# Optimization experiments

Hardware: AMD Instinct MI355X
Metric: run time of the kernel (lower is better)

## Reference

```python
import jax, jax.numpy as jnp
import numpy as np

B, N, F_IN = 4, 8000, 256
D_DIST = 128   # distance_dim
DFF = 128      # hidden width of both FFNs
BIN_SIZE = 500
NBINS = N // BIN_SIZE  # 16
K = 8          # num_neighbors
DIST_MULT = 0.1
MAX_NUM_BINS = 200


def setup_inputs() -> dict:
    key = jax.random.key(0)
    ks = jax.random.split(key, 8)
    s = 0.05
    return {
        "inputs": jax.random.normal(ks[0], (B, N, F_IN), jnp.float32),
        "enc_w1": jax.random.normal(ks[1], (F_IN, DFF), jnp.float32) * s,
        "enc_b1": jnp.zeros((DFF,), jnp.float32),
        "enc_w2": jax.random.normal(ks[2], (DFF, D_DIST), jnp.float32) * s,
        "enc_b2": jnp.zeros((D_DIST,), jnp.float32),
        "edge_w1": jax.random.normal(ks[3], (2 * F_IN + 1, DFF), jnp.float32) * s,
        "edge_b1": jnp.zeros((DFF,), jnp.float32),
        "edge_w2": jax.random.normal(ks[4], (DFF, 1), jnp.float32) * s,
        "edge_b2": jnp.zeros((1,), jnp.float32),
        "rot": jax.random.normal(ks[5], (D_DIST, MAX_NUM_BINS // 2), jnp.float32) * 0.05,
    }


def _per_batch(points, rot):
    # points: [N, D_DIST]. LSH bucketing via random rotations.
    mul = points @ rot[:, : NBINS // 2]                 # [N, NBINS//2]
    cmul = jnp.concatenate([mul, -mul], axis=-1)        # [N, NBINS]
    bin_idx = jnp.argmax(cmul, axis=-1)
    bins_split = jnp.argsort(bin_idx).astype(jnp.int32).reshape(NBINS, BIN_SIZE)
    parts = points[bins_split]                          # [NBINS, BIN_SIZE, D]
    # per-bin pairwise gaussian kernel
    na = jnp.sum(parts * parts, axis=-1)                # [NBINS, BIN_SIZE]
    d2 = na[:, :, None] - 2.0 * jnp.einsum('bnd,bmd->bnm', parts, parts) + na[:, None, :]
    dm = jnp.exp(-DIST_MULT * jnp.sqrt(jnp.maximum(d2, 1e-6)))  # [NBINS, BS, BS]
    vals, idx = jax.lax.top_k(dm, K)                    # [NBINS, BS, K]
    dst = jax.vmap(lambda b, i: b[i])(bins_split, idx)  # map in-bin idx -> global
    src = jnp.broadcast_to(bins_split[:, :, None], dst.shape)
    return src.reshape(-1), dst.reshape(-1), vals.reshape(-1), bins_split


def reference(inputs, enc_w1, enc_b1, enc_w2, enc_b2,
              edge_w1, edge_b1, edge_w2, edge_b2, rot):
    # point encoding FFN: Dense(128, elu) -> Dense(distance_dim)
    pe = jax.nn.elu(inputs @ enc_w1 + enc_b1) @ enc_w2 + enc_b2  # [B, N, D_DIST]
    src, dst, vals, bins_split = jax.vmap(_per_batch, in_axes=(0, None))(pe, rot)
    bidx = jnp.broadcast_to(jnp.arange(B, dtype=jnp.int32)[:, None], src.shape)
    src = src.reshape(-1)
    dst = dst.reshape(-1)
    vals = vals.reshape(-1)
    bidx = bidx.reshape(-1)
    # tf.sparse.reorder: canonical row-major ordering (no duplicates: top-k
    # indices are distinct per row and src is unique per neighbor slot)
    order = jnp.lexsort((dst, src, bidx))
    bidx, src, dst, vals = bidx[order], src[order], dst[order], vals[order]
    # edge network on gathered endpoint features + kernel value
    x1 = inputs[bidx, src]                               # [E, F_IN]
    x2 = inputs[bidx, dst]
    e = jnp.concatenate([x1, x2, vals[:, None]], axis=-1)  # [E, 2*F_IN+1]
    edge_vals = jax.nn.sigmoid(jax.nn.elu(e @ edge_w1 + edge_b1) @ edge_w2 + edge_b2)[:, 0]
    indices = jnp.stack([bidx, src, dst], axis=-1)       # [E, 3] sparse indices
    return indices, edge_vals, bins_split
```

## Files before the change

### kernel.cpp

```cpp
#include <hip/hip_runtime.h>
#include <math.h>

#define BB 4
#define NN 8000
#define FIN 256
#define DD 128
#define NB 16
#define BS 500
#define KK 8
#define RPB 32
#define CHUNKS (NN/RPB)
#define ETOT (BB*NN*KK)

__global__ __launch_bounds__(256) void k_fused(
    const float* __restrict__ x, const float* __restrict__ w1, const float* __restrict__ b1,
    const float* __restrict__ w2, const float* __restrict__ b2, const float* __restrict__ rot,
    const float* __restrict__ ew1,
    float* __restrict__ pe, float* __restrict__ A, float* __restrict__ Bv,
    int* __restrict__ bin_idx, int* __restrict__ localrank, int* __restrict__ chunkhist)
{
  __shared__ float wsa[32*132];
  __shared__ float wsb[32*132];
  __shared__ float ps[RPB*132];
  __shared__ float ms[RPB*9];
  __shared__ int   bl[RPB];
  const int t = threadIdx.x;
  const int b = blockIdx.x / CHUNKS;
  const int chunk = blockIdx.x % CHUNKS;
  const int row0 = chunk * RPB;
  const int ri = t >> 4;
  const int ci = t & 15;
  const int r0t = ri*2, r1t = ri*2+1;
  const float* xrow0 = x + ((size_t)b*NN + row0 + r0t)*FIN;
  const float* xrow1 = x + ((size_t)b*NN + row0 + r1t)*FIN;
  const int sk = t >> 5, sc4 = t & 31;

  float acc0[8], acc1[8];
  #pragma unroll
  for (int j=0;j<8;j++){ float bb = b1[ci*8+j]; acc0[j]=bb; acc1[j]=bb; }

  float4 rw0,rw1,rw2,rw3;
  { const float4* wg = (const float4*)w1;
    rw0=wg[t]; rw1=wg[t+256]; rw2=wg[t+512]; rw3=wg[t+768]; }
  int cur = 0;
  for (int kt=0; kt<8; ++kt){
    float* wsc = cur ? wsb : wsa;
    *(float4*)&wsc[(sk   )*132 + sc4*4] = rw0;
    *(float4*)&wsc[(sk+ 8)*132 + sc4*4] = rw1;
    *(float4*)&wsc[(sk+16)*132 + sc4*4] = rw2;
    *(float4*)&wsc[(sk+24)*132 + sc4*4] = rw3;
    if (kt<7){ const float4* wg = (const float4*)(w1 + (size_t)(kt+1)*32*DD);
      rw0=wg[t]; rw1=wg[t+256]; rw2=wg[t+512]; rw3=wg[t+768]; }
    __syncthreads();
    const float* xp0 = xrow0 + kt*32;
    const float* xp1 = xrow1 + kt*32;
    #pragma unroll
    for (int kc=0;kc<32;kc+=4){
      float4 a0 = *(const float4*)(xp0+kc);
      float4 a1 = *(const float4*)(xp1+kc);
      #pragma unroll
      for (int kk=0;kk<4;kk++){
        float4 wlo = *(const float4*)&wsc[(kc+kk)*132 + ci*8];
        float4 whi = *(const float4*)&wsc[(kc+kk)*132 + ci*8 + 4];
        float a0v = ((const float*)&a0)[kk], a1v = ((const float*)&a1)[kk];
        acc0[0]=fmaf(a0v,wlo.x,acc0[0]); acc0[1]=fmaf(a0v,wlo.y,acc0[1]);
        acc0[2]=fmaf(a0v,wlo.z,acc0[2]); acc0[3]=fmaf(a0v,wlo.w,acc0[3]);
        acc0[4]=fmaf(a0v,whi.x,acc0[4]); acc0[5]=fmaf(a0v,whi.y,acc0[5]);
        acc0[6]=fmaf(a0v,whi.z,acc0[6]); acc0[7]=fmaf(a0v,whi.w,acc0[7]);
        acc1[0]=fmaf(a1v,wlo.x,acc1[0]); acc1[1]=fmaf(a1v,wlo.y,acc1[1]);
        acc1[2]=fmaf(a1v,wlo.z,acc1[2]); acc1[3]=fmaf(a1v,wlo.w,acc1[3]);
        acc1[4]=fmaf(a1v,whi.x,acc1[4]); acc1[5]=fmaf(a1v,whi.y,acc1[5]);
        acc1[6]=fmaf(a1v,whi.z,acc1[6]); acc1[7]=fmaf(a1v,whi.w,acc1[7]);
      }
    }
    cur ^= 1;
  }
  #pragma unroll
  for (int j=0;j<8;j++){
    float v0=acc0[j]; ps[r0t*132 + ci*8 + j] = v0>0.f ? v0 : expm1f(v0);
    float v1=acc1[j]; ps[r1t*132 + ci*8 + j] = v1>0.f ? v1 : expm1f(v1);
  }

  float acc20[8], acc21[8];
  #pragma unroll
  for (int j=0;j<8;j++){ float bb = b2[ci*8+j]; acc20[j]=bb; acc21[j]=bb; }
  { const float4* wg = (const float4*)w2;
    rw0=wg[t]; rw1=wg[t+256]; rw2=wg[t+512]; rw3=wg[t+768]; }
  for (int kt=0; kt<4; ++kt){
    float* wsc = cur ? wsb : wsa;
    *(float4*)&wsc[(sk   )*132 + sc4*4] = rw0;
    *(float4*)&wsc[(sk+ 8)*132 + sc4*4] = rw1;
    *(float4*)&wsc[(sk+16)*132 + sc4*4] = rw2;
    *(float4*)&wsc[(sk+24)*132 + sc4*4] = rw3;
    if (kt<3){ const float4* wg = (const float4*)(w2 + (size_t)(kt+1)*32*DD);
      rw0=wg[t]; rw1=wg[t+256]; rw2=wg[t+512]; rw3=wg[t+768]; }
    __syncthreads();
    #pragma unroll
    for (int kc=0;kc<32;kc+=4){
      float4 a0 = *(const float4*)&ps[r0t*132 + kt*32 + kc];
      float4 a1 = *(const float4*)&ps[r1t*132 + kt*32 + kc];
      #pragma unroll
      for (int kk=0;kk<4;kk++){
        float4 wlo = *(const float4*)&wsc[(kc+kk)*132 + ci*8];
        float4 whi = *(const float4*)&wsc[(kc+kk)*132 + ci*8 + 4];
        float a0v = ((const float*)&a0)[kk], a1v = ((const float*)&a1)[kk];
        acc20[0]=fmaf(a0v,wlo.x,acc20[0]); acc20[1]=fmaf(a0v,wlo.y,acc20[1]);
        acc20[2]=fmaf(a0v,wlo.z,acc20[2]); acc20[3]=fmaf(a0v,wlo.w,acc20[3]);
        acc20[4]=fmaf(a0v,whi.x,acc20[4]); acc20[5]=fmaf(a0v,whi.y,acc20[5]);
        acc20[6]=fmaf(a0v,whi.z,acc20[6]); acc20[7]=fmaf(a0v,whi.w,acc20[7]);
        acc21[0]=fmaf(a1v,wlo.x,acc21[0]); acc21[1]=fmaf(a1v,wlo.y,acc21[1]);
        acc21[2]=fmaf(a1v,wlo.z,acc21[2]); acc21[3]=fmaf(a1v,wlo.w,acc21[3]);
        acc21[4]=fmaf(a1v,whi.x,acc21[4]); acc21[5]=fmaf(a1v,whi.y,acc21[5]);
        acc21[6]=fmaf(a1v,whi.z,acc21[6]); acc21[7]=fmaf(a1v,whi.w,acc21[7]);
      }
    }
    cur ^= 1;
  }
  __syncthreads();

  { float* pg0 = pe + ((size_t)b*NN + row0 + r0t)*DD + ci*8;
    float* pg1 = pe + ((size_t)b*NN + row0 + r1t)*DD + ci*8;
    #pragma unroll
    for (int j=0;j<8;j+=4){
      float4 v0 = make_float4(acc20[j],acc20[j+1],acc20[j+2],acc20[j+3]);
      float4 v1 = make_float4(acc21[j],acc21[j+1],acc21[j+2],acc21[j+3]);
      *(float4*)(pg0+j)=v0; *(float4*)&ps[r0t*132 + ci*8 + j]=v0;
      *(float4*)(pg1+j)=v1; *(float4*)&ps[r1t*132 + ci*8 + j]=v1;
    } }

  float aA0[8], aA1[8], aB0[8], aB1[8];
  #pragma unroll
  for (int j=0;j<8;j++){ aA0[j]=0.f; aA1[j]=0.f; aB0[j]=0.f; aB1[j]=0.f; }
  float4 ra0,ra1,ra2,ra3, rb0,rb1,rb2,rb3;
  { const float4* wga = (const float4*)ew1;
    const float4* wgb = (const float4*)(ew1 + (size_t)FIN*DD);
    ra0=wga[t]; ra1=wga[t+256]; ra2=wga[t+512]; ra3=wga[t+768];
    rb0=wgb[t]; rb1=wgb[t+256]; rb2=wgb[t+512]; rb3=wgb[t+768]; }
  for (int kt=0; kt<8; ++kt){
    __syncthreads();
    *(float4*)&wsa[(sk   )*132 + sc4*4] = ra0;
    *(float4*)&wsa[(sk+ 8)*132 + sc4*4] = ra1;
    *(float4*)&wsa[(sk+16)*132 + sc4*4] = ra2;
    *(float4*)&wsa[(sk+24)*132 + sc4*4] = ra3;
    *(float4*)&wsb[(sk   )*132 + sc4*4] = rb0;
    *(float4*)&wsb[(sk+ 8)*132 + sc4*4] = rb1;
    *(float4*)&wsb[(sk+16)*132 + sc4*4] = rb2;
    *(float4*)&wsb[(sk+24)*132 + sc4*4] = rb3;
    if (kt<7){
      const float4* wga = (const float4*)(ew1 + (size_t)(kt+1)*32*DD);
      const float4* wgb = (const float4*)(ew1 + (size_t)(FIN + (kt+1)*32)*DD);
      ra0=wga[t]; ra1=wga[t+256]; ra2=wga[t+512]; ra3=wga[t+768];
      rb0=wgb[t]; rb1=wgb[t+256]; rb2=wgb[t+512]; rb3=wgb[t+768]; }
    __syncthreads();
    const float* xp0 = xrow0 + kt*32;
    const float* xp1 = xrow1 + kt*32;
    #pragma unroll
    for (int kc=0;kc<32;kc+=4){
      float4 a0 = *(const float4*)(xp0+kc);
      float4 a1 = *(const float4*)(xp1+kc);
      #pragma unroll
      for (int kk=0;kk<4;kk++){
        float4 alo = *(const float4*)&wsa[(kc+kk)*132 + ci*8];
        float4 ahi = *(const float4*)&wsa[(kc+kk)*132 + ci*8 + 4];
        float4 blo = *(const float4*)&wsb[(kc+kk)*132 + ci*8];
        float4 bhi = *(const float4*)&wsb[(kc+kk)*132 + ci*8 + 4];
        float a0v = ((const float*)&a0)[kk], a1v = ((const float*)&a1)[kk];
        aA0[0]=fmaf(a0v,alo.x,aA0[0]); aA0[1]=fmaf(a0v,alo.y,aA0[1]);
        aA0[2]=fmaf(a0v,alo.z,aA0[2]); aA0[3]=fmaf(a0v,alo.w,aA0[3]);
        aA0[4]=fmaf(a0v,ahi.x,aA0[4]); aA0[5]=fmaf(a0v,ahi.y,aA0[5]);
        aA0[6]=fmaf(a0v,ahi.z,aA0[6]); aA0[7]=fmaf(a0v,ahi.w,aA0[7]);
        aA1[0]=fmaf(a1v,alo.x,aA1[0]); aA1[1]=fmaf(a1v,alo.y,aA1[1]);
        aA1[2]=fmaf(a1v,alo.z,aA1[2]); aA1[3]=fmaf(a1v,alo.w,aA1[3]);
        aA1[4]=fmaf(a1v,ahi.x,aA1[4]); aA1[5]=fmaf(a1v,ahi.y,aA1[5]);
        aA1[6]=fmaf(a1v,ahi.z,aA1[6]); aA1[7]=fmaf(a1v,ahi.w,aA1[7]);
        aB0[0]=fmaf(a0v,blo.x,aB0[0]); aB0[1]=fmaf(a0v,blo.y,aB0[1]);
        aB0[2]=fmaf(a0v,blo.z,aB0[2]); aB0[3]=fmaf(a0v,blo.w,aB0[3]);
        aB0[4]=fmaf(a0v,bhi.x,aB0[4]); aB0[5]=fmaf(a0v,bhi.y,aB0[5]);
        aB0[6]=fmaf(a0v,bhi.z,aB0[6]); aB0[7]=fmaf(a0v,bhi.w,aB0[7]);
        aB1[0]=fmaf(a1v,blo.x,aB1[0]); aB1[1]=fmaf(a1v,blo.y,aB1[1]);
        aB1[2]=fmaf(a1v,blo.z,aB1[2]); aB1[3]=fmaf(a1v,blo.w,aB1[3]);
        aB1[4]=fmaf(a1v,bhi.x,aB1[4]); aB1[5]=fmaf(a1v,bhi.y,aB1[5]);
        aB1[6]=fmaf(a1v,bhi.z,aB1[6]); aB1[7]=fmaf(a1v,bhi.w,aB1[7]);
      }
    }
  }
  { float* Ag0 = A  + ((size_t)b*NN+row0+r0t)*DD + ci*8;
    float* Ag1 = A  + ((size_t)b*NN+row0+r1t)*DD + ci*8;
    float* Bg0 = Bv + ((size_t)b*NN+row0+r0t)*DD + ci*8;
    float* Bg1 = Bv + ((size_t)b*NN+row0+r1t)*DD + ci*8;
    #pragma unroll
    for (int j=0;j<8;j+=4){
      *(float4*)(Ag0+j)=make_float4(aA0[j],aA0[j+1],aA0[j+2],aA0[j+3]);
      *(float4*)(Ag1+j)=make_float4(aA1[j],aA1[j+1],aA1[j+2],aA1[j+3]);
      *(float4*)(Bg0+j)=make_float4(aB0[j],aB0[j+1],aB0[j+2],aB0[j+3]);
      *(float4*)(Bg1+j)=make_float4(aB1[j],aB1[j+1],aB1[j+2],aB1[j+3]);
    } }

  if (t<128){
    const int r = t>>2, m0 = t&3;
    float s0=0.f, s1=0.f;
    for (int k=0;k<DD;k++){
      float p = ps[r*132+k];
      s0 = fmaf(p, rot[k*100+m0],   s0);
      s1 = fmaf(p, rot[k*100+m0+4], s1);
    }
    ms[r*9+m0]=s0; ms[r*9+m0+4]=s1;
  }
  __syncthreads();
  if (t<RPB){
    float best = ms[t*9+0]; int bi=0;
    #pragma unroll
    for (int m=1;m<16;m++){
      float v = (m<8)? ms[t*9+m] : -ms[t*9+(m-8)];
      if (v>best){best=v;bi=m;}
    }
    bl[t]=bi;
    bin_idx[b*NN+row0+t]=bi;
  }
  __syncthreads();
  if (t<RPB){
    int myb=bl[t]; int rk=0;
    for (int r2=0;r2<t;r2++) rk += (bl[r2]==myb) ? 1 : 0;
    localrank[b*NN+row0+t]=rk;
  }
  if (t<NB){
    int cnt=0;
    #pragma unroll
    for (int r2=0;r2<RPB;r2++) cnt += (bl[r2]==t) ? 1 : 0;
    chunkhist[(b*CHUNKS+chunk)*NB + t] = cnt;
  }
}

__global__ __launch_bounds__(256) void k_scan_scatter(
    const int* __restrict__ bin_idx, const int* __restrict__ localrank,
    const int* __restrict__ chunkhist, int* __restrict__ bs, float* __restrict__ out_bins)
{
  const int b=blockIdx.x, t=threadIdx.x;
  __shared__ int cbase_s[CHUNKS*NB];
  __shared__ int segsum[16*NB];
  __shared__ int start[NB];
  const int m = t&15, s = t>>4;
  const int c0 = s*16, c1 = min(c0+16, CHUNKS);
  { int run=0;
    for (int c=c0;c<c1;c++) run += chunkhist[(b*CHUNKS+c)*NB+m];
    segsum[s*NB+m]=run; }
  __syncthreads();
  if (t<NB){
    int acc=0;
    for (int s2=0;s2<16;s2++){ int v=segsum[s2*NB+t]; segsum[s2*NB+t]=acc; acc+=v; }
    start[t]=acc;
  }
  __syncthreads();
  if (t==0){
    int run=0;
    for (int mm=0;mm<NB;mm++){ int tt=start[mm]; start[mm]=run; run+=tt; }
  }
  __syncthreads();
  { int acc = start[m] + segsum[s*NB+m];
    for (int c=c0;c<c1;c++){
      cbase_s[c*NB+m]=acc;
      acc += chunkhist[(b*CHUNKS+c)*NB+m];
    } }
  __syncthreads();
  for (int row=t; row<NN; row+=256){
    int gi=b*NN+row;
    int chunk=row>>5;
    int bi=bin_idx[gi];
    int pos=cbase_s[chunk*NB+bi]+localrank[gi];
    bs[b*NN+pos]=row;
    out_bins[b*NN+pos]=(float)row;
  }
}

__global__ __launch_bounds__(256) void k_nn(
    const float* __restrict__ pe, const int* __restrict__ bs,
    float* __restrict__ out_idx, int* __restrict__ e_dst, float* __restrict__ e_val)
{
  __shared__ float RT[64*132];
  __shared__ float CT[64*132];
  __shared__ float na_all[512];
  __shared__ int   bsl[BS];
  const int t=threadIdx.x;
  const int blk=blockIdx.x;
  const int rt=blk&7, bin=(blk>>3)&15, b=blk>>7;

  for (int i=t;i<BS;i+=256) bsl[i]=bs[b*NN + bin*BS + i];
  __syncthreads();

  for (int i=t;i<BS;i+=256){
    const float* pr = pe + ((size_t)b*NN + bsl[i])*DD;
    float s=0.f;
    for (int k=0;k<DD;k+=4){
      float4 v=*(const float4*)(pr+k);
      s=fmaf(v.x,v.x,s); s=fmaf(v.y,v.y,s); s=fmaf(v.z,v.z,s); s=fmaf(v.w,v.w,s);
    }
    na_all[i]=s;
  }

  const int r0=rt*64;
  const int nr=min(64, BS-r0);
  const int lr=t>>5, c4=t&31;
  #pragma unroll
  for (int pass=0;pass<8;pass++){
    int r=pass*8+lr;
    float4 v=make_float4(0.f,0.f,0.f,0.f);
    if (r<nr) v=*(const float4*)(pe + ((size_t)b*NN + bsl[r0+r])*DD + c4*4);
    *(float4*)&RT[r*132 + c4*4] = v;
  }
  float4 creg[8];
  #pragma unroll
  for (int pass=0;pass<8;pass++){
    int c=pass*8+lr;
    creg[pass]=*(const float4*)(pe + ((size_t)b*NN + bsl[c])*DD + c4*4);
  }
  __syncthreads();
  #pragma unroll
  for (int pass=0;pass<8;pass++){
    int c=pass*8+lr; int swz=((c>>3)&3)<<2;
    *(float4*)&CT[c*132 + ((c4*4) ^ swz)] = creg[pass];
  }
  __syncthreads();

  float tv[4][8]; int tix[4][8];
  #pragma unroll
  for (int i=0;i<4;i++){
    #pragma unroll
    for (int s=0;s<8;s++){ tv[i][s]=-1e30f; tix[i][s]=0; } }

  const int tr_=t>>4, tc_=t&15;
  const int cswz = ((tc_>>1)&3)<<2;

  for (int ct=0; ct<8; ++ct){
    const int c0=ct*64;
    if (ct<7){
      const int c0n=c0+64;
      const int ncn=min(64, BS-c0n);
      #pragma unroll
      for (int pass=0;pass<8;pass++){
        int c=pass*8+lr;
        creg[pass]=make_float4(0.f,0.f,0.f,0.f);
        if (c<ncn) creg[pass]=*(const float4*)(pe + ((size_t)b*NN + bsl[c0n+c])*DD + c4*4);
      }
    }

    float accm[4][4];
    #pragma unroll
    for (int i=0;i<4;i++){
      #pragma unroll
      for (int j=0;j<4;j++) accm[i][j]=0.f; }
    #pragma unroll 8
    for (int k0=0;k0<DD;k0+=4){
      float4 a4[4], b4[4];
      #pragma unroll
      for (int i=0;i<4;i++) a4[i]=*(const float4*)&RT[(tr_*4+i)*132 + k0];
      #pragma unroll
      for (int j=0;j<4;j++) b4[j]=*(const float4*)&CT[(tc_*4+j)*132 + (k0 ^ cswz)];
      #pragma unroll
      for (int kk=0;kk<4;kk++){
        #pragma unroll
        for (int i=0;i<4;i++){
          float av=((const float*)&a4[i])[kk];
          #pragma unroll
          for (int j=0;j<4;j++){
            float bvv=((const float*)&b4[j])[kk];
            accm[i][j]=fmaf(av,bvv,accm[i][j]);
          }
        }
      }
    }

    float nrow[4], ncol[4];
    #pragma unroll
    for (int i=0;i<4;i++) nrow[i]=na_all[r0+tr_*4+i];
    #pragma unroll
    for (int j=0;j<4;j++) ncol[j]=na_all[c0+tc_*4+j];

    #pragma unroll
    for (int i=0;i<4;i++){
      #pragma unroll
      for (int j=0;j<4;j++){
        float t1=nrow[i]-2.f*accm[i][j];
        float d2v=t1+ncol[j];
        float dm=expf(-0.1f*sqrtf(fmaxf(d2v,1e-6f)));
        int c=c0+tc_*4+j;
        if (c<BS && dm>tv[i][7]){
          tv[i][7]=dm; tix[i][7]=c;
          #pragma unroll
          for (int q=7;q>0;q--){
            if (tv[i][q]>tv[i][q-1]){
              float tf=tv[i][q];tv[i][q]=tv[i][q-1];tv[i][q-1]=tf;
              int   td=tix[i][q];tix[i][q]=tix[i][q-1];tix[i][q-1]=td;
            }
          }
        }
      }
    }
    __syncthreads();
    if (ct<7){
      #pragma unroll
      for (int pass=0;pass<8;pass++){
        int c=pass*8+lr; int swz=((c>>3)&3)<<2;
        *(float4*)&CT[c*132 + ((c4*4) ^ swz)] = creg[pass];
      }
      __syncthreads();
    }
  }

  #pragma unroll
  for (int i=0;i<4;i++){
    const int row=tr_*4+i;
    #pragma unroll
    for (int s=0;s<8;s++){
      const int p=tc_*8+s;
      RT[p*65 + row]=tv[i][s];
      CT[p*65 + row]=__int_as_float(tix[i][s]);
    }
  }
  __syncthreads();

  if (t<nr){
    float mv[8]; int mi[8];
    #pragma unroll
    for (int s=0;s<8;s++){ mv[s]=-1e30f; mi[s]=0; }
    #pragma unroll 4
    for (int p=0;p<128;p++){
      float v=RT[p*65+t]; int c=__float_as_int(CT[p*65+t]);
      if (v>mv[7] || (v==mv[7] && c<mi[7])){
        mv[7]=v; mi[7]=c;
        #pragma unroll
        for (int q=7;q>0;q--){
          bool sw=(mv[q]>mv[q-1]) || (mv[q]==mv[q-1] && mi[q]<mi[q-1]);
          if (sw){
            float tf=mv[q];mv[q]=mv[q-1];mv[q-1]=tf;
            int   td=mi[q];mi[q]=mi[q-1];mi[q-1]=td;
          }
        }
      }
    }
    const int src=bsl[r0+t];
    int dsts[KK]; float vv[KK];
    #pragma unroll
    for (int k2=0;k2<KK;k2++){ dsts[k2]=bsl[mi[k2]]; vv[k2]=mv[k2]; }
    #define CSWAP(a_,b_) { if (dsts[a_]>dsts[b_]){ int td=dsts[a_];dsts[a_]=dsts[b_];dsts[b_]=td; float tf=vv[a_];vv[a_]=vv[b_];vv[b_]=tf; } }
    CSWAP(0,1) CSWAP(2,3) CSWAP(4,5) CSWAP(6,7)
    CSWAP(0,2) CSWAP(1,3) CSWAP(4,6) CSWAP(5,7)
    CSWAP(1,2) CSWAP(5,6)
    CSWAP(0,4) CSWAP(1,5) CSWAP(2,6) CSWAP(3,7)
    CSWAP(2,4) CSWAP(3,5)
    CSWAP(1,2) CSWAP(3,4) CSWAP(5,6)
    #undef CSWAP
    size_t e0=((size_t)b*NN + src)*KK;
    #pragma unroll
    for (int k2=0;k2<KK;k2++){
      out_idx[3*(e0+k2)+0]=(float)b;
      out_idx[3*(e0+k2)+1]=(float)src;
      out_idx[3*(e0+k2)+2]=(float)dsts[k2];
      e_dst[e0+k2]=dsts[k2];
      e_val[e0+k2]=vv[k2];
    }
  }
}

__global__ __launch_bounds__(256) void k_edge(
    const float* __restrict__ A, const float* __restrict__ Bv,
    const float* __restrict__ ew1, const float* __restrict__ eb1,
    const float* __restrict__ ew2, const float* __restrict__ eb2,
    const int* __restrict__ e_dst, const float* __restrict__ e_val,
    float* __restrict__ out_vals)
{
  const int wid = (int)((blockIdx.x*256u+threadIdx.x)>>6);
  const int lane = threadIdx.x&63;
  if (wid >= BB*NN) return;
  const int b = wid / NN;
  const float2 a2  = *(const float2*)(A   + (size_t)wid*DD + lane*2);
  const float2 wc  = *(const float2*)(ew1 + (size_t)512*DD + lane*2);
  const float2 bb1 = *(const float2*)(eb1 + lane*2);
  const float2 w2v = *(const float2*)(ew2 + lane*2);
  const float  b2s = eb2[0];
  const size_t e0 = (size_t)wid*KK;
  #pragma unroll
  for (int k=0;k<KK;k++){
    int dst = e_dst[e0+k];
    float val = e_val[e0+k];
    const float2 bv = *(const float2*)(Bv + ((size_t)b*NN+dst)*DD + lane*2);
    float h0 = a2.x + bv.x + val*wc.x + bb1.x;  h0 = h0>0.f ? h0 : expm1f(h0);
    float h1 = a2.y + bv.y + val*wc.y + bb1.y;  h1 = h1>0.f ? h1 : expm1f(h1);
    float s = h0*w2v.x + h1*w2v.y;
    #pragma unroll
    for (int off=32; off; off>>=1) s += __shfl_xor(s, off);
    if (lane==k) out_vals[e0+k] = 1.f/(1.f+expf(-(s+b2s)));
  }
}

extern "C" void kernel_launch(void* const* d_in, const int* in_sizes, int n_in,
                              void* d_out, int out_size, void* d_ws, size_t ws_size,
                              hipStream_t stream)
{
  const float* x    = (const float*)d_in[0];
  const float* ew1v = (const float*)d_in[1];
  const float* eb1v = (const float*)d_in[2];
  const float* ew2v = (const float*)d_in[3];
  const float* eb2v = (const float*)d_in[4];
  const float* gw1  = (const float*)d_in[5];
  const float* gb1  = (const float*)d_in[6];
  const float* gw2  = (const float*)d_in[7];
  const float* gb2  = (const float*)d_in[8];
  const float* rot  = (const float*)d_in[9];

  char* w = (char*)d_ws;
  float* pe   = (float*)w;  w += (size_t)BB*NN*DD*4;
  float* Atab = (float*)w;  w += (size_t)BB*NN*DD*4;
  float* Btab = (float*)w;  w += (size_t)BB*NN*DD*4;
  int*   bin_idx   = (int*)w; w += (size_t)BB*NN*4;
  int*   localrank = (int*)w; w += (size_t)BB*NN*4;
  int*   chunkhist = (int*)w; w += (size_t)BB*CHUNKS*NB*4;
  int*   bs        = (int*)w; w += (size_t)BB*NN*4;
  int*   e_dst     = (int*)w; w += (size_t)ETOT*4;
  float* e_val     = (float*)w; w += (size_t)ETOT*4;

  float* out_idx  = (float*)d_out;
  float* out_vals = out_idx + (size_t)ETOT*3;
  float* out_bins = out_vals + ETOT;

  k_fused<<<dim3(BB*CHUNKS), dim3(256), 0, stream>>>(
      x, ew1v, eb1v, ew2v, eb2v, rot, gw1,
      pe, Atab, Btab, bin_idx, localrank, chunkhist);
  k_scan_scatter<<<dim3(BB), dim3(256), 0, stream>>>(
      bin_idx, localrank, chunkhist, bs, out_bins);
  k_nn<<<dim3(BB*NB*8), dim3(256), 0, stream>>>(pe, bs, out_idx, e_dst, e_val);
  k_edge<<<dim3(BB*NN/4), dim3(256), 0, stream>>>(
      Atab, Btab, gw1, gb1, gw2, gb2, e_dst, e_val, out_vals);
}
```

Measured before the change: 514.4 us.

## Give each wave a private column tile in pairwise kernel and pad LDS weight writes

```diff
diff --git a/kernel.cpp b/kernel.cpp
--- a/kernel.cpp
+++ b/kernel.cpp
@@ -34,6 +34,8 @@
   const float* xrow0 = x + ((size_t)b*NN + row0 + r0t)*FIN;
   const float* xrow1 = x + ((size_t)b*NN + row0 + r1t)*FIN;
   const int sk = t >> 5, sc4 = t & 31;
+  const int ss = (sc4>>4)<<2;
+  const int cs = (ci>>3)<<2;
 
   float acc0[8], acc1[8];
   #pragma unroll
@@ -45,10 +47,10 @@
   int cur = 0;
   for (int kt=0; kt<8; ++kt){
     float* wsc = cur ? wsb : wsa;
-    *(float4*)&wsc[(sk   )*132 + sc4*4] = rw0;
-    *(float4*)&wsc[(sk+ 8)*132 + sc4*4] = rw1;
-    *(float4*)&wsc[(sk+16)*132 + sc4*4] = rw2;
-    *(float4*)&wsc[(sk+24)*132 + sc4*4] = rw3;
+    *(float4*)&wsc[(sk   )*132 + sc4*4 + ss] = rw0;
+    *(float4*)&wsc[(sk+ 8)*132 + sc4*4 + ss] = rw1;
+    *(float4*)&wsc[(sk+16)*132 + sc4*4 + ss] = rw2;
+    *(float4*)&wsc[(sk+24)*132 + sc4*4 + ss] = rw3;
     if (kt<7){ const float4* wg = (const float4*)(w1 + (size_t)(kt+1)*32*DD);
       rw0=wg[t]; rw1=wg[t+256]; rw2=wg[t+512]; rw3=wg[t+768]; }
     __syncthreads();
@@ -60,8 +62,8 @@
       float4 a1 = *(const float4*)(xp1+kc);
       #pragma unroll
       for (int kk=0;kk<4;kk++){
-        float4 wlo = *(const float4*)&wsc[(kc+kk)*132 + ci*8];
-        float4 whi = *(const float4*)&wsc[(kc+kk)*132 + ci*8 + 4];
+        float4 wlo = *(const float4*)&wsc[(kc+kk)*132 + ci*8 + cs];
+        float4 whi = *(const float4*)&wsc[(kc+kk)*132 + ci*8 + 4 + cs];
         float a0v = ((const float*)&a0)[kk], a1v = ((const float*)&a1)[kk];
         acc0[0]=fmaf(a0v,wlo.x,acc0[0]); acc0[1]=fmaf(a0v,wlo.y,acc0[1]);
         acc0[2]=fmaf(a0v,wlo.z,acc0[2]); acc0[3]=fmaf(a0v,wlo.w,acc0[3]);
@@ -88,10 +90,10 @@
     rw0=wg[t]; rw1=wg[t+256]; rw2=wg[t+512]; rw3=wg[t+768]; }
   for (int kt=0; kt<4; ++kt){
     float* wsc = cur ? wsb : wsa;
-    *(float4*)&wsc[(sk   )*132 + sc4*4] = rw0;
-    *(float4*)&wsc[(sk+ 8)*132 + sc4*4] = rw1;
-    *(float4*)&wsc[(sk+16)*132 + sc4*4] = rw2;
-    *(float4*)&wsc[(sk+24)*132 + sc4*4] = rw3;
+    *(float4*)&wsc[(sk   )*132 + sc4*4 + ss] = rw0;
+    *(float4*)&wsc[(sk+ 8)*132 + sc4*4 + ss] = rw1;
+    *(float4*)&wsc[(sk+16)*132 + sc4*4 + ss] = rw2;
+    *(float4*)&wsc[(sk+24)*132 + sc4*4 + ss] = rw3;
     if (kt<3){ const float4* wg = (const float4*)(w2 + (size_t)(kt+1)*32*DD);
       rw0=wg[t]; rw1=wg[t+256]; rw2=wg[t+512]; rw3=wg[t+768]; }
     __syncthreads();
@@ -101,8 +103,8 @@
       float4 a1 = *(const float4*)&ps[r1t*132 + kt*32 + kc];
       #pragma unroll
       for (int kk=0;kk<4;kk++){
-        float4 wlo = *(const float4*)&wsc[(kc+kk)*132 + ci*8];
-        float4 whi = *(const float4*)&wsc[(kc+kk)*132 + ci*8 + 4];
+        float4 wlo = *(const float4*)&wsc[(kc+kk)*132 + ci*8 + cs];
+        float4 whi = *(const float4*)&wsc[(kc+kk)*132 + ci*8 + 4 + cs];
         float a0v = ((const float*)&a0)[kk], a1v = ((const float*)&a1)[kk];
         acc20[0]=fmaf(a0v,wlo.x,acc20[0]); acc20[1]=fmaf(a0v,wlo.y,acc20[1]);
         acc20[2]=fmaf(a0v,wlo.z,acc20[2]); acc20[3]=fmaf(a0v,wlo.w,acc20[3]);
@@ -138,14 +140,14 @@
     rb0=wgb[t]; rb1=wgb[t+256]; rb2=wgb[t+512]; rb3=wgb[t+768]; }
   for (int kt=0; kt<8; ++kt){
     __syncthreads();
-    *(float4*)&wsa[(sk   )*132 + sc4*4] = ra0;
-    *(float4*)&wsa[(sk+ 8)*132 + sc4*4] = ra1;
-    *(float4*)&wsa[(sk+16)*132 + sc4*4] = ra2;
-    *(float4*)&wsa[(sk+24)*132 + sc4*4] = ra3;
-    *(float4*)&wsb[(sk   )*132 + sc4*4] = rb0;
-    *(float4*)&wsb[(sk+ 8)*132 + sc4*4] = rb1;
-    *(float4*)&wsb[(sk+16)*132 + sc4*4] = rb2;
-    *(float4*)&wsb[(sk+24)*132 + sc4*4] = rb3;
+    *(float4*)&wsa[(sk   )*132 + sc4*4 + ss] = ra0;
+    *(float4*)&wsa[(sk+ 8)*132 + sc4*4 + ss] = ra1;
+    *(float4*)&wsa[(sk+16)*132 + sc4*4 + ss] = ra2;
+    *(float4*)&wsa[(sk+24)*132 + sc4*4 + ss] = ra3;
+    *(float4*)&wsb[(sk   )*132 + sc4*4 + ss] = rb0;
+    *(float4*)&wsb[(sk+ 8)*132 + sc4*4 + ss] = rb1;
+    *(float4*)&wsb[(sk+16)*132 + sc4*4 + ss] = rb2;
+    *(float4*)&wsb[(sk+24)*132 + sc4*4 + ss] = rb3;
     if (kt<7){
       const float4* wga = (const float4*)(ew1 + (size_t)(kt+1)*32*DD);
       const float4* wgb = (const float4*)(ew1 + (size_t)(FIN + (kt+1)*32)*DD);
@@ -160,10 +162,10 @@
       float4 a1 = *(const float4*)(xp1+kc);
       #pragma unroll
       for (int kk=0;kk<4;kk++){
-        float4 alo = *(const float4*)&wsa[(kc+kk)*132 + ci*8];
-        float4 ahi = *(const float4*)&wsa[(kc+kk)*132 + ci*8 + 4];
-        float4 blo = *(const float4*)&wsb[(kc+kk)*132 + ci*8];
-        float4 bhi = *(const float4*)&wsb[(kc+kk)*132 + ci*8 + 4];
+        float4 alo = *(const float4*)&wsa[(kc+kk)*132 + ci*8 + cs];
+        float4 ahi = *(const float4*)&wsa[(kc+kk)*132 + ci*8 + 4 + cs];
+        float4 blo = *(const float4*)&wsb[(kc+kk)*132 + ci*8 + cs];
+        float4 bhi = *(const float4*)&wsb[(kc+kk)*132 + ci*8 + 4 + cs];
         float a0v = ((const float*)&a0)[kk], a1v = ((const float*)&a1)[kk];
         aA0[0]=fmaf(a0v,alo.x,aA0[0]); aA0[1]=fmaf(a0v,alo.y,aA0[1]);
         aA0[2]=fmaf(a0v,alo.z,aA0[2]); aA0[3]=fmaf(a0v,alo.w,aA0[3]);
@@ -277,49 +279,54 @@
     float* __restrict__ out_idx, int* __restrict__ e_dst, float* __restrict__ e_val)
 {
   __shared__ float RT[64*132];
-  __shared__ float CT[64*132];
+  __shared__ float CT[4*16*132];
   __shared__ float na_all[512];
   __shared__ int   bsl[BS];
   const int t=threadIdx.x;
   const int blk=blockIdx.x;
   const int rt=blk&7, bin=(blk>>3)&15, b=blk>>7;
+  const int w = t>>6, lane = t&63;
+  const int tr = lane>>2, tc = lane&3;
+  const float* peb = pe + (size_t)b*NN*DD;
 
   for (int i=t;i<BS;i+=256) bsl[i]=bs[b*NN + bin*BS + i];
   __syncthreads();
 
-  for (int i=t;i<BS;i+=256){
-    const float* pr = pe + ((size_t)b*NN + bsl[i])*DD;
+  for (int i=t;i<512;i+=256){
     float s=0.f;
-    for (int k=0;k<DD;k+=4){
-      float4 v=*(const float4*)(pr+k);
-      s=fmaf(v.x,v.x,s); s=fmaf(v.y,v.y,s); s=fmaf(v.z,v.z,s); s=fmaf(v.w,v.w,s);
+    if (i<BS){
+      const float* pr = peb + (size_t)bsl[i]*DD;
+      for (int k=0;k<DD;k+=4){
+        float4 v=*(const float4*)(pr+k);
+        s=fmaf(v.x,v.x,s); s=fmaf(v.y,v.y,s); s=fmaf(v.z,v.z,s); s=fmaf(v.w,v.w,s);
+      }
     }
     na_all[i]=s;
   }
 
   const int r0=rt*64;
   const int nr=min(64, BS-r0);
-  const int lr=t>>5, c4=t&31;
-  #pragma unroll
-  for (int pass=0;pass<8;pass++){
-    int r=pass*8+lr;
-    float4 v=make_float4(0.f,0.f,0.f,0.f);
-    if (r<nr) v=*(const float4*)(pe + ((size_t)b*NN + bsl[r0+r])*DD + c4*4);
-    *(float4*)&RT[r*132 + c4*4] = v;
-  }
+  { const int lr=t>>5, c4=t&31;
+    #pragma unroll
+    for (int pass=0;pass<8;pass++){
+      int r=pass*8+lr;
+      float4 v=make_float4(0.f,0.f,0.f,0.f);
+      if (r<nr) v=*(const float4*)(peb + (size_t)bsl[r0+r]*DD + c4*4);
+      *(float4*)&RT[r*132 + ((c4*4) ^ (((r>>2)&7)<<2))] = v;
+    } }
+
+  const int scol = lane>>2, sch = lane&3;
+  float* ctw = CT + w*(16*132);
   float4 creg[8];
-  #pragma unroll
-  for (int pass=0;pass<8;pass++){
-    int c=pass*8+lr;
-    creg[pass]=*(const float4*)(pe + ((size_t)b*NN + bsl[c])*DD + c4*4);
-  }
-  __syncthreads();
-  #pragma unroll
-  for (int pass=0;pass<8;pass++){
-    int c=pass*8+lr; int swz=((c>>3)&3)<<2;
-    *(float4*)&CT[c*132 + ((c4*4) ^ swz)] = creg[pass];
-  }
-  __syncthreads();
+  { const float* src = peb + (size_t)bsl[w*16 + scol]*DD;
+    #pragma unroll
+    for (int p=0;p<8;p++) creg[p]=*(const float4*)(src + (sch+4*p)*4);
+  }
+  __syncthreads();
+
+  #pragma unroll
+  for (int p=0;p<8;p++)
+    *(float4*)&ctw[scol*132 + (sch+4*p)*4] = creg[p];
 
   float tv[4][8]; int tix[4][8];
   #pragma unroll
@@ -327,19 +334,17 @@
     #pragma unroll
     for (int s=0;s<8;s++){ tv[i][s]=-1e30f; tix[i][s]=0; } }
 
-  const int tr_=t>>4, tc_=t&15;
-  const int cswz = ((tc_>>1)&3)<<2;
-
-  for (int ct=0; ct<8; ++ct){
-    const int c0=ct*64;
-    if (ct<7){
-      const int c0n=c0+64;
-      const int ncn=min(64, BS-c0n);
-      #pragma unroll
-      for (int pass=0;pass<8;pass++){
-        int c=pass*8+lr;
-        creg[pass]=make_float4(0.f,0.f,0.f,0.f);
-        if (c<ncn) creg[pass]=*(const float4*)(pe + ((size_t)b*NN + bsl[c0n+c])*DD + c4*4);
+  const int aswz = (tr&7)<<2;
+
+  for (int q=0;q<8;q++){
+    const int c0 = (4*q + w)*16;
+    if (q<7){
+      int cn = c0 + 64 + scol;
+      const float* src = peb + (size_t)bsl[(cn<BS)?cn:0]*DD;
+      #pragma unroll
+      for (int p=0;p<8;p++){
+        float4 v=*(const float4*)(src + (sch+4*p)*4);
+        creg[p] = (cn<BS) ? v : make_float4(0.f,0.f,0.f,0.f);
       }
     }
 
@@ -352,9 +357,9 @@
     for (int k0=0;k0<DD;k0+=4){
       float4 a4[4], b4[4];
       #pragma unroll
-      for (int i=0;i<4;i++) a4[i]=*(const float4*)&RT[(tr_*4+i)*132 + k0];
-      #pragma unroll
-      for (int j=0;j<4;j++) b4[j]=*(const float4*)&CT[(tc_*4+j)*132 + (k0 ^ cswz)];
+      for (int i=0;i<4;i++) a4[i]=*(const float4*)&RT[(tr*4+i)*132 + (k0 ^ aswz)];
+      #pragma unroll
+      for (int j=0;j<4;j++) b4[j]=*(const float4*)&ctw[(tc*4+j)*132 + k0];
       #pragma unroll
       for (int kk=0;kk<4;kk++){
         #pragma unroll
@@ -371,9 +376,9 @@
 
     float nrow[4], ncol[4];
     #pragma unroll
-    for (int i=0;i<4;i++) nrow[i]=na_all[r0+tr_*4+i];
-    #pragma unroll
-    for (int j=0;j<4;j++) ncol[j]=na_all[c0+tc_*4+j];
+    for (int i=0;i<4;i++) nrow[i]=na_all[r0+tr*4+i];
+    #pragma unroll
+    for (int j=0;j<4;j++) ncol[j]=na_all[c0+tc*4+j];
 
     #pragma unroll
     for (int i=0;i<4;i++){
@@ -382,36 +387,34 @@
         float t1=nrow[i]-2.f*accm[i][j];
         float d2v=t1+ncol[j];
         float dm=expf(-0.1f*sqrtf(fmaxf(d2v,1e-6f)));
-        int c=c0+tc_*4+j;
+        int c=c0+tc*4+j;
         if (c<BS && dm>tv[i][7]){
           tv[i][7]=dm; tix[i][7]=c;
           #pragma unroll
-          for (int q=7;q>0;q--){
-            if (tv[i][q]>tv[i][q-1]){
-              float tf=tv[i][q];tv[i][q]=tv[i][q-1];tv[i][q-1]=tf;
-              int   td=tix[i][q];tix[i][q]=tix[i][q-1];tix[i][q-1]=td;
+          for (int qq=7;qq>0;qq--){
+            if (tv[i][qq]>tv[i][qq-1]){
+              float tf=tv[i][qq];tv[i][qq]=tv[i][qq-1];tv[i][qq-1]=tf;
+              int   td=tix[i][qq];tix[i][qq]=tix[i][qq-1];tix[i][qq-1]=td;
             }
           }
         }
       }
     }
-    __syncthreads();
-    if (ct<7){
-      #pragma unroll
-      for (int pass=0;pass<8;pass++){
-        int c=pass*8+lr; int swz=((c>>3)&3)<<2;
-        *(float4*)&CT[c*132 + ((c4*4) ^ swz)] = creg[pass];
-      }
-      __syncthreads();
-    }
-  }
-
+
+    if (q<7){
+      #pragma unroll
+      for (int p=0;p<8;p++)
+        *(float4*)&ctw[scol*132 + (sch+4*p)*4] = creg[p];
+    }
+  }
+
+  __syncthreads();
   #pragma unroll
   for (int i=0;i<4;i++){
-    const int row=tr_*4+i;
+    const int row=tr*4+i;
     #pragma unroll
     for (int s=0;s<8;s++){
-      const int p=tc_*8+s;
+      const int p=(w*4+tc)*8+s;
       RT[p*65 + row]=tv[i][s];
       CT[p*65 + row]=__int_as_float(tix[i][s]);
     }
@@ -428,11 +431,11 @@
       if (v>mv[7] || (v==mv[7] && c<mi[7])){
         mv[7]=v; mi[7]=c;
         #pragma unroll
-        for (int q=7;q>0;q--){
-          bool sw=(mv[q]>mv[q-1]) || (mv[q]==mv[q-1] && mi[q]<mi[q-1]);
+        for (int qq=7;qq>0;qq--){
+          bool sw=(mv[qq]>mv[qq-1]) || (mv[qq]==mv[qq-1] && mi[qq]<mi[qq-1]);
           if (sw){
-            float tf=mv[q];mv[q]=mv[q-1];mv[q-1]=tf;
-            int   td=mi[q];mi[q]=mi[q-1];mi[q-1]=td;
+            float tf=mv[qq];mv[qq]=mv[qq-1];mv[qq-1]=tf;
+            int   td=mi[qq];mi[qq]=mi[qq-1];mi[qq-1]=td;
           }
         }
       }
```

New measurement: 503.1 us. 1.02x faster.
